# Kernel optimization log

Hardware: AMD Instinct MI355X
Metric: run time of the kernel (lower is better)

## Reference

```python
import jax, jax.numpy as jnp
import numpy as np

GS, GL, LS, LL, NA = 8, 8, 16, 8, 12
ALPHA = 0.5


def _rgb_to_lab(img):
    # img: (B,3,H,W) in [0,1]. Standard sRGB -> CIELab (kornia convention).
    lin = jnp.where(img > 0.04045, ((img + 0.055) / 1.055) ** 2.4, img / 12.92)
    r, g, b = lin[:, 0], lin[:, 1], lin[:, 2]
    x = 0.412453 * r + 0.357580 * g + 0.180423 * b
    y = 0.212671 * r + 0.715160 * g + 0.072169 * b
    z = 0.019334 * r + 0.119193 * g + 0.950227 * b
    xn, yn, zn = x / 0.950456, y, z / 1.088754
    f = lambda t: jnp.where(t > 0.008856, jnp.cbrt(t), 7.787 * t + 4.0 / 29.0)
    fx, fy, fz = f(xn), f(yn), f(zn)
    L = 116.0 * fy - 16.0
    a = 500.0 * (fx - fy)
    bb = 200.0 * (fy - fz)
    return L, a, bb


def _bilateral_slice(grid, img, guide):
    # grid: (B,12,s,s,l); img: (B,3,H,W); guide: (B,H,W) in [0,1]
    B, C, s, _, l = grid.shape
    _, _, H, W = img.shape
    g5 = jnp.transpose(grid, (0, 4, 2, 3, 1))  # (B, D=l, Hg=s, Wg=s, C)
    # align_corners=True coordinates, border padding == clamp
    fx = jnp.linspace(0.0, s - 1.0, W)                    # (W,)
    fy = jnp.linspace(0.0, s - 1.0, H)                    # (H,)
    fz = jnp.clip(guide * (l - 1.0), 0.0, l - 1.0)        # (B,H,W)
    x0 = jnp.floor(fx).astype(jnp.int32); x1 = jnp.minimum(x0 + 1, s - 1)
    y0 = jnp.floor(fy).astype(jnp.int32); y1 = jnp.minimum(y0 + 1, s - 1)
    z0 = jnp.floor(fz).astype(jnp.int32); z1 = jnp.minimum(z0 + 1, l - 1)
    wx = (fx - x0)[None, None, :, None]
    wy = (fy - y0)[None, :, None, None]
    wz = (fz - z0)[..., None]
    bi = jnp.arange(B)[:, None, None]
    yi0, yi1 = y0[None, :, None], y1[None, :, None]
    xi0, xi1 = x0[None, None, :], x1[None, None, :]

    def gat(zi, yi, xi):
        return g5[bi, zi, yi, xi]  # (B,H,W,C)

    def bilin(zi):
        c00 = gat(zi, yi0, xi0) * (1 - wx) + gat(zi, yi0, xi1) * wx
        c10 = gat(zi, yi1, xi0) * (1 - wx) + gat(zi, yi1, xi1) * wx
        return c00 * (1 - wy) + c10 * wy

    coeffs = bilin(z0) * (1 - wz) + bilin(z1) * wz       # (B,H,W,12)
    A = coeffs[..., :9].reshape(B, H, W, 3, 3)
    bvec = coeffs[..., 9:]
    img_hwc = jnp.transpose(img, (0, 2, 3, 1))           # (B,H,W,3)
    out = jnp.einsum('bhwck,bhwk->bhwc', A, img_hwc) + bvec
    return jnp.transpose(jnp.clip(out, 0.0, 1.0), (0, 3, 1, 2))


def setup_inputs() -> dict:
    key = jax.random.key(0)
    ks = jax.random.split(key, 16)
    B, H, W = 4, 896, 896
    n_h = n_w = 64
    inp = {
        'R_spatial': jax.random.normal(ks[0], (B, 256, n_h, n_w), jnp.float32),
        'F_sem': jax.random.normal(ks[1], (B, n_h * n_w, 384), jnp.float32),
        'img': jax.random.uniform(ks[2], (B, 3, H, W), jnp.float32),
        'n_h': n_h,
        'n_w': n_w,
    }
    sc = 0.02
    identity = np.array([1., 0., 0., 0., 1., 0., 0., 0., 1., 0., 0., 0.], np.float32)
    inp['dino_proj_w'] = jax.random.normal(ks[3], (128, 384), jnp.float32) * sc
    inp['dino_proj_b'] = jnp.zeros((128,), jnp.float32)
    inp['fusion_w'] = jax.random.normal(ks[4], (256, 384), jnp.float32) * sc
    inp['fusion_b'] = jnp.zeros((256,), jnp.float32)
    inp['g1_w'] = jax.random.normal(ks[5], (256, 256), jnp.float32) * sc
    inp['g1_b'] = jnp.zeros((256,), jnp.float32)
    inp['g2_w'] = jax.random.normal(ks[6], (NA * GS * GS * GL, 256), jnp.float32) * sc
    inp['g2_b'] = jnp.asarray(np.repeat(identity, GS * GS * GL))  # identity init
    inp['local_w'] = jax.random.normal(ks[7], (NA * LL, 256), jnp.float32) * sc
    inp['local_b'] = jnp.asarray(np.repeat(identity, LL))
    inp['guide_w1'] = jax.random.normal(ks[8], (64, 384), jnp.float32) * sc
    inp['guide_b1'] = jnp.zeros((64,), jnp.float32)
    inp['guide_w2'] = jax.random.normal(ks[9], (1, 64), jnp.float32) * sc
    inp['guide_b2'] = jnp.zeros((1,), jnp.float32)
    return inp


def reference(R_spatial, F_sem, img, n_h, n_w,
              dino_proj_w, dino_proj_b, fusion_w, fusion_b,
              g1_w, g1_b, g2_w, g2_b, local_w, local_b,
              guide_w1, guide_b1, guide_w2, guide_b2):
    B, _, H, W = img.shape
    # ---- GridNet ----
    F_sp = jnp.transpose(F_sem, (0, 2, 1)).reshape(B, 384, n_h, n_w)
    proj = jnp.einsum('bchw,oc->bohw', F_sp, dino_proj_w) + dino_proj_b[None, :, None, None]
    fused_in = jnp.concatenate([R_spatial, proj], axis=1)
    fused = jnp.einsum('bchw,oc->bohw', fused_in, fusion_w) + fusion_b[None, :, None, None]
    f_gap = fused.mean(axis=(-2, -1))                       # (B,256)
    h = jax.nn.relu(f_gap @ g1_w.T + g1_b)
    G_global = (h @ g2_w.T + g2_b).reshape(B, NA, GS, GS, GL)
    kh, kw = n_h // LS, n_w // LS
    pooled = fused.reshape(B, 256, LS, kh, LS, kw).mean(axis=(3, 5))
    lflat = jnp.einsum('bchw,oc->bohw', pooled, local_w) + local_b[None, :, None, None]
    G_local = jnp.transpose(lflat.reshape(B, NA, LL, LS, LS), (0, 1, 3, 4, 2))
    # ---- SemanticGuide ----
    L, a, bb = _rgb_to_lab(img)
    g_chroma = jnp.clip((0.5 * L + 0.25 * jnp.abs(a) + 0.25 * jnp.abs(bb)) / 114.0, 0.0, 1.0)
    hsem = jax.nn.relu(jnp.einsum('bnd,hd->bnh', F_sem, guide_w1) + guide_b1)
    g_sem_patch = jax.nn.sigmoid(jnp.einsum('bnh,oh->bno', hsem, guide_w2) + guide_b2)
    g_sem_patch = g_sem_patch.reshape(B, n_h, n_w, 1).transpose(0, 3, 1, 2)
    g_sem = jax.image.resize(g_sem_patch, (B, 1, H, W), 'bilinear')[:, 0]
    g = ALPHA * g_chroma + (1.0 - ALPHA) * g_sem
    # ---- slice + apply ----
    I_global = _bilateral_slice(G_global, img, g)
    I_local = _bilateral_slice(G_local, img, g)
    return I_global, I_local, G_global, G_local, g
```

## Files before the change

kernel.cpp:

```cpp
#include <hip/hip_runtime.h>
#include <math.h>

#define HWPIX 802816
#define OUT_IL 9633792
#define OUT_GG 19267584
#define OUT_GL 19292160
#define OUT_G  19390464

#define WS_WT4  0
#define WS_BC   163840
#define WS_POOL 164096
#define WS_H    426240
#define WS_GSEM 427264
#define WS_RG   443648
#define WS_RL   468224
#define WS_W1T  566528
#define WS_LWT  591104

__device__ __forceinline__ float fast_exp2(float x) {
  return __builtin_amdgcn_exp2f(x);
}
__device__ __forceinline__ float fast_log2(float x) {
  return __builtin_amdgcn_logf(x);
}
__device__ __forceinline__ float srgb_lin(float v) {
  float p = fast_exp2(2.4f * fast_log2((v + 0.055f) * (1.0f / 1.055f)));
  return v > 0.04045f ? p : v * (1.0f / 12.92f);
}
__device__ __forceinline__ float labf(float t) {
  float c = fast_exp2((1.0f / 3.0f) * fast_log2(t));
  return t > 0.008856f ? c : 7.787f * t + (4.0f / 29.0f);
}

__global__ __launch_bounds__(256) void k_prep(
    const float* __restrict__ fus_w, const float* __restrict__ fus_b,
    const float* __restrict__ dino_w, const float* __restrict__ dino_b,
    const float* __restrict__ gw1, const float* __restrict__ lw,
    float* __restrict__ Wt4, float* __restrict__ bc, float* __restrict__ w1T,
    float* __restrict__ lwT) {
  if (blockIdx.x == 642) {
    int t = threadIdx.x;
    for (int it = 0; it < 96; ++it) {
      int idx = it * 256 + t;
      int o = idx >> 8;
      int c = idx & 255;
      lwT[c * 96 + o] = lw[o * 256 + c];
    }
    return;
  }
  if (blockIdx.x == 641) {
    int t = threadIdx.x;
    for (int it = 0; it < 96; ++it) {
      int idx = it * 256 + t;
      int h = idx & 63;
      int k = idx >> 6;
      int kq = k / 96;
      int krem = k - kq * 96;
      int k4 = krem >> 2;
      int j = krem & 3;
      int hg = h >> 4, hl = h & 15;
      w1T[((((kq * 24 + k4) * 4 + hg) * 16) + hl) * 4 + j] = gw1[h * 384 + k];
    }
    return;
  }
  if (blockIdx.x == 640) {
    int o = threadIdx.x;
    float acc = fus_b[o];
    for (int m = 0; m < 128; ++m) acc += fus_w[o * 384 + 256 + m] * dino_b[m];
    bc[o] = acc;
    return;
  }
  int idx = blockIdx.x * 256 + threadIdx.x;
  int o = idx / 640;
  int k = idx - o * 640;
  float val;
  if (k < 256) {
    val = fus_w[o * 384 + k];
  } else {
    int d = k - 256;
    float acc = 0.0f;
    for (int m = 0; m < 128; ++m)
      acc += fus_w[o * 384 + 256 + m] * dino_w[m * 384 + d];
    val = acc;
  }
  Wt4[((k >> 2) * 256 + o) * 4 + (k & 3)] = val;
}

__global__ __launch_bounds__(1024) void k_fused_pool(
    const float* __restrict__ R, const float* __restrict__ F,
    const float* __restrict__ Wt4, const float* __restrict__ bc,
    const float* __restrict__ lwT, const float* __restrict__ lb,
    float* __restrict__ pooled, float* __restrict__ out4,
    float* __restrict__ rl) {
  int blk = blockIdx.x;
  int b = blk >> 6;
  int i = (blk >> 2) & 15;
  int jg = blk & 3;
  int t = threadIdx.x;
  int cell = t >> 8;
  int c = t & 255;
  __shared__ float s[4 * 640];
  {
    const float* rb = R + (((b * 256 + c) * 64 + i * 4) * 64) + (jg * 4 + cell) * 4;
    float p = 0.0f;
#pragma unroll
    for (int di = 0; di < 4; ++di) {
      float4 v = *(const float4*)(rb + di * 64);
      p += v.x + v.y + v.z + v.w;
    }
    s[cell * 640 + c] = p;
  }
  {
    float a0 = 0.0f, a1 = 0.0f;
    const float* fb = F + (size_t)(b * 4096 + (i * 4) * 64 + (jg * 4 + cell) * 4) * 384;
#pragma unroll
    for (int pix = 0; pix < 16; ++pix) {
      const float* fr = fb + (size_t)((pix >> 2) * 64 + (pix & 3)) * 384;
      a0 += fr[c];
      if (c < 128) a1 += fr[256 + c];
    }
    s[cell * 640 + 256 + c] = a0;
    if (c < 128) s[cell * 640 + 512 + c] = a1;
  }
  __syncthreads();
  float acc = 0.0f;
  const float4* w4 = (const float4*)Wt4;
  const float4* s4 = (const float4*)(s + cell * 640);
#pragma unroll 8
  for (int kk = 0; kk < 160; ++kk) {
    float4 wv = w4[kk * 256 + c];
    float4 sv = s4[kk];
    acc += wv.x * sv.x + wv.y * sv.y + wv.z * sv.z + wv.w * sv.w;
  }
  __syncthreads();
  s[cell * 256 + c] = acc;
  __syncthreads();
  if (t < 256) {
    float bco = bc[t];
    float4 v;
    v.x = s[0 * 256 + t] * (1.0f / 16.0f) + bco;
    v.y = s[1 * 256 + t] * (1.0f / 16.0f) + bco;
    v.z = s[2 * 256 + t] * (1.0f / 16.0f) + bco;
    v.w = s[3 * 256 + t] * (1.0f / 16.0f) + bco;
    *(float4*)(pooled + ((size_t)(b * 256 + t) * 256) + i * 16 + jg * 4) = v;
  } else if (t < 640) {
    int idx = t - 256;
    int cl = idx / 96;
    int o = idx - cl * 96;
    const float* sc_ = s + cl * 256;
    float acc2 = lb[o];
    for (int cc = 0; cc < 256; ++cc) {
      float pv = sc_[cc] * (1.0f / 16.0f) + bc[cc];
      acc2 += lwT[cc * 96 + o] * pv;
    }
    int cellg = i * 16 + jg * 4 + cl;
    int n = o >> 3, l = o & 7;
    out4[((b * 12 + n) * 256 + cellg) * 8 + l] = acc2;
    rl[b * 24576 + (cellg * 8 + l) * 12 + n] = acc2;
  }
}

__global__ __launch_bounds__(1024) void k_head(
    const float* __restrict__ pooled, const float* __restrict__ g1_w,
    const float* __restrict__ g1_b, const float* __restrict__ g2_w,
    const float* __restrict__ g2_b, float* __restrict__ out3,
    float* __restrict__ rg) {
  int b = blockIdx.x / 24;
  int og = (blockIdx.x % 24) * 256;
  int t = threadIdx.x;
  int ol = t & 255;
  int q = t >> 8;
  __shared__ float part[4][256];
  __shared__ float f[256];
  __shared__ float hv[256];
  {
    const float4* pr4 = (const float4*)(pooled + (size_t)(b * 256 + ol) * 256 + q * 64);
    float s = 0.0f;
#pragma unroll
    for (int i = 0; i < 16; ++i) {
      float4 v = pr4[i];
      s += v.x + v.y + v.z + v.w;
    }
    part[q][ol] = s;
  }
  __syncthreads();
  if (t < 256)
    f[t] = (part[0][t] + part[1][t] + part[2][t] + part[3][t]) * (1.0f / 256.0f);
  __syncthreads();
  {
    const float4* wr = (const float4*)(g1_w + (size_t)ol * 256 + q * 64);
    const float4* fq = (const float4*)(f + q * 64);
    float acc = 0.0f;
#pragma unroll
    for (int i = 0; i < 16; ++i) {
      float4 w = wr[i];
      float4 v = fq[i];
      acc += w.x * v.x + w.y * v.y + w.z * v.z + w.w * v.w;
    }
    part[q][ol] = acc;
  }
  __syncthreads();
  if (t < 256)
    hv[t] = fmaxf(part[0][t] + part[1][t] + part[2][t] + part[3][t] + g1_b[t], 0.0f);
  __syncthreads();
  {
    const float4* wr = (const float4*)(g2_w + (size_t)(og + ol) * 256 + q * 64);
    const float4* hq = (const float4*)(hv + q * 64);
    float acc = 0.0f;
#pragma unroll
    for (int i = 0; i < 16; ++i) {
      float4 w = wr[i];
      float4 v = hq[i];
      acc += w.x * v.x + w.y * v.y + w.z * v.z + w.w * v.w;
    }
    part[q][ol] = acc;
  }
  __syncthreads();
  if (t < 256) {
    int o = og + t;
    float a = part[0][t] + part[1][t] + part[2][t] + part[3][t] + g2_b[o];
    out3[b * 6144 + o] = a;
    int n = o >> 9, y = (o >> 6) & 7, x = (o >> 3) & 7, z = o & 7;
    rg[b * 6144 + ((y * 8 + x) * 8 + z) * 12 + n] = a;
  }
}

__global__ __launch_bounds__(256) void k_guide(
    const float* __restrict__ F, const float* __restrict__ w1T,
    const float* __restrict__ b1, const float* __restrict__ w2,
    const float* __restrict__ b2, float* __restrict__ gsem) {
  int t = threadIdx.x;
  int wave = t >> 6;
  int lane = t & 63;
  int kq = lane >> 4;
  int hl = lane & 15;
  int pb = blockIdx.x * 16;
  __shared__ float4 sF[16 * 4 * 25];
  const float4* Fb = (const float4*)(F + (size_t)pb * 384);
#pragma unroll
  for (int r6 = 0; r6 < 6; ++r6) {
    int g = r6 * 256 + t;
    int row = g / 96;
    int col = g - row * 96;
    int cq = col / 24;
    int c4 = col - cq * 24;
    sF[(row * 4 + cq) * 25 + c4] = Fb[g];
  }
  __syncthreads();
  float acc[4][4];
#pragma unroll
  for (int p = 0; p < 4; ++p)
#pragma unroll
    for (int hg = 0; hg < 4; ++hg) acc[p][hg] = 0.0f;
  const float4* w4 = (const float4*)w1T;
  int prow = wave * 4;
  for (int k4 = 0; k4 < 24; ++k4) {
    float4 wv0 = w4[((kq * 24 + k4) * 4 + 0) * 16 + hl];
    float4 wv1 = w4[((kq * 24 + k4) * 4 + 1) * 16 + hl];
    float4 wv2 = w4[((kq * 24 + k4) * 4 + 2) * 16 + hl];
    float4 wv3 = w4[((kq * 24 + k4) * 4 + 3) * 16 + hl];
#pragma unroll
    for (int p = 0; p < 4; ++p) {
      float4 fv = sF[((prow + p) * 4 + kq) * 25 + k4];
      acc[p][0] += fv.x * wv0.x + fv.y * wv0.y + fv.z * wv0.z + fv.w * wv0.w;
      acc[p][1] += fv.x * wv1.x + fv.y * wv1.y + fv.z * wv1.z + fv.w * wv1.w;
      acc[p][2] += fv.x * wv2.x + fv.y * wv2.y + fv.z * wv2.z + fv.w * wv2.w;
      acc[p][3] += fv.x * wv3.x + fv.y * wv3.y + fv.z * wv3.z + fv.w * wv3.w;
    }
  }
#pragma unroll
  for (int p = 0; p < 4; ++p)
#pragma unroll
    for (int hg = 0; hg < 4; ++hg) {
      float v = acc[p][hg];
      v += __shfl_xor(v, 16, 64);
      v += __shfl_xor(v, 32, 64);
      acc[p][hg] = v;
    }
  float b1v[4], w2v[4];
#pragma unroll
  for (int hg = 0; hg < 4; ++hg) {
    b1v[hg] = b1[hg * 16 + hl];
    w2v[hg] = w2[hg * 16 + hl];
  }
  float b2v = b2[0];
  float res = 0.0f;
#pragma unroll
  for (int p = 0; p < 4; ++p) {
    float v = 0.0f;
#pragma unroll
    for (int hg = 0; hg < 4; ++hg)
      v += fmaxf(acc[p][hg] + b1v[hg], 0.0f) * w2v[hg];
#pragma unroll
    for (int m = 8; m >= 1; m >>= 1) v += __shfl_xor(v, m, 64);
    if (lane == p) res = v;
  }
  if (lane < 4) gsem[pb + prow + lane] = 1.0f / (1.0f + expf(-(res + b2v)));
}

template <int SDIM>
__device__ __forceinline__ void slice_lds(
    const float* __restrict__ sg, int w, int z0, int z1, float wz,
    float r, float g, float bl, float& o0, float& o1, float& o2) {
  constexpr float sc = (float)(SDIM - 1) * (1.0f / 895.0f);
  float fxs = (float)w * sc;
  int x0 = (int)fxs;
  if (x0 > SDIM - 1) x0 = SDIM - 1;
  int x1 = x0 < SDIM - 1 ? x0 + 1 : SDIM - 1;
  float wx = fxs - (float)x0;
  float wz0 = 1.0f - wz;
  float w00 = (1.0f - wx) * wz0;
  float w01 = (1.0f - wx) * wz;
  float w10 = wx * wz0;
  float w11 = wx * wz;
  const float4* p00 = (const float4*)(sg + (x0 * 8 + z0) * 12);
  const float4* p01 = (const float4*)(sg + (x0 * 8 + z1) * 12);
  const float4* p10 = (const float4*)(sg + (x1 * 8 + z0) * 12);
  const float4* p11 = (const float4*)(sg + (x1 * 8 + z1) * 12);
  float a[12];
#pragma unroll
  for (int c = 0; c < 3; ++c) {
    float4 v00 = p00[c], v01 = p01[c], v10 = p10[c], v11 = p11[c];
    a[4 * c + 0] = w00 * v00.x + w01 * v01.x + w10 * v10.x + w11 * v11.x;
    a[4 * c + 1] = w00 * v00.y + w01 * v01.y + w10 * v10.y + w11 * v11.y;
    a[4 * c + 2] = w00 * v00.z + w01 * v01.z + w10 * v10.z + w11 * v11.z;
    a[4 * c + 3] = w00 * v00.w + w01 * v01.w + w10 * v10.w + w11 * v11.w;
  }
  o0 = fminf(fmaxf(a[0] * r + a[1] * g + a[2] * bl + a[9], 0.0f), 1.0f);
  o1 = fminf(fmaxf(a[3] * r + a[4] * g + a[5] * bl + a[10], 0.0f), 1.0f);
  o2 = fminf(fmaxf(a[6] * r + a[7] * g + a[8] * bl + a[11], 0.0f), 1.0f);
}

__global__ __launch_bounds__(448) void k_pixel(
    const float* __restrict__ img, const float* __restrict__ gsem,
    const float* __restrict__ rg, const float* __restrict__ rl,
    float* __restrict__ out) {
  int blk = blockIdx.x;
  int b = blk / 896;
  int h = blk - b * 896;
  int t = threadIdx.x;
  __shared__ float sgr[64];
  __shared__ float sG[768];
  __shared__ float sL[1536];

  int hwA = h * 896 + t;
  int hwB = hwA + 448;
  const float* imb = img + (size_t)b * 3 * HWPIX;
  float rrA = imb[hwA],             rrB = imb[hwB];
  float ggA = imb[HWPIX + hwA],     ggB = imb[HWPIX + hwB];
  float bbA = imb[2 * HWPIX + hwA], bbB = imb[2 * HWPIX + hwB];

  float sy = fminf(fmaxf((h + 0.5f) * (1.0f / 14.0f) - 0.5f, 0.0f), 63.0f);
  int y0s = (int)sy;
  int y1s = y0s < 63 ? y0s + 1 : 63;
  float wys = sy - (float)y0s;
  float fyg = (float)h * (7.0f / 895.0f);
  int y0g = (int)fyg;
  if (y0g > 7) y0g = 7;
  int y1g = y0g < 7 ? y0g + 1 : 7;
  float wyg = fyg - (float)y0g;
  float fyl = (float)h * (15.0f / 895.0f);
  int y0l = (int)fyl;
  if (y0l > 15) y0l = 15;
  int y1l = y0l < 15 ? y0l + 1 : 15;
  float wyl = fyl - (float)y0l;

  const float* g0 = rg + b * 6144 + y0g * 768;
  const float* g1 = rg + b * 6144 + y1g * 768;
  const float* l0 = rl + b * 24576 + y0l * 1536;
  const float* l1 = rl + b * 24576 + y1l * 1536;
  float ga0 = g0[t], gb0 = g1[t];
  float ga1 = 0.0f, gb1 = 0.0f;
  if (t < 320) { ga1 = g0[t + 448]; gb1 = g1[t + 448]; }
  float la0 = l0[t], lb0 = l1[t];
  float la1 = l0[t + 448], lb1 = l1[t + 448];
  float la2 = l0[t + 896], lb2s = l1[t + 896];
  float la3 = 0.0f, lb3 = 0.0f;
  if (t < 192) { la3 = l0[t + 1344]; lb3 = l1[t + 1344]; }
  float sg0 = 0.0f, sg1 = 0.0f;
  if (t < 64) {
    const float* gbp = gsem + b * 4096;
    sg0 = gbp[y0s * 64 + t];
    sg1 = gbp[y1s * 64 + t];
  }
  sG[t] = ga0 * (1.0f - wyg) + gb0 * wyg;
  if (t < 320) sG[t + 448] = ga1 * (1.0f - wyg) + gb1 * wyg;
  sL[t] = la0 * (1.0f - wyl) + lb0 * wyl;
  sL[t + 448] = la1 * (1.0f - wyl) + lb1 * wyl;
  sL[t + 896] = la2 * (1.0f - wyl) + lb2s * wyl;
  if (t < 192) sL[t + 1344] = la3 * (1.0f - wyl) + lb3 * wyl;
  if (t < 64) sgr[t] = sg0 * (1.0f - wys) + sg1 * wys;
  __syncthreads();

  float rr_[2] = {rrA, rrB}, gg_[2] = {ggA, ggB}, bb_[2] = {bbA, bbB};
#pragma unroll
  for (int ip = 0; ip < 2; ++ip) {
    int w = ip * 448 + t;
    int hw = h * 896 + w;
    float r = rr_[ip];
    float g = gg_[ip];
    float bl = bb_[ip];
    float lr = srgb_lin(r), lg = srgb_lin(g), lb2 = srgb_lin(bl);
    float X = 0.412453f * lr + 0.357580f * lg + 0.180423f * lb2;
    float Y = 0.212671f * lr + 0.715160f * lg + 0.072169f * lb2;
    float Z = 0.019334f * lr + 0.119193f * lg + 0.950227f * lb2;
    float fx_ = labf(X * (1.0f / 0.950456f));
    float fy_ = labf(Y);
    float fz_ = labf(Z * (1.0f / 1.088754f));
    float gch = 0.50877193f * fy_ - 0.070175439f +
                1.0964912f * fabsf(fx_ - fy_) + 0.43859649f * fabsf(fy_ - fz_);
    gch = fminf(fmaxf(gch, 0.0f), 1.0f);
    float sx = fminf(fmaxf((w + 0.5f) * (1.0f / 14.0f) - 0.5f, 0.0f), 63.0f);
    int x0s = (int)sx;
    int x1s = x0s < 63 ? x0s + 1 : 63;
    float wxs = sx - (float)x0s;
    float gs = sgr[x0s] * (1.0f - wxs) + sgr[x1s] * wxs;
    float gg = 0.5f * gch + 0.5f * gs;
    __builtin_nontemporal_store(gg, &out[OUT_G + b * HWPIX + hw]);
    float fzc = fminf(fmaxf(gg * 7.0f, 0.0f), 7.0f);
    int z0 = (int)fzc;
    if (z0 > 7) z0 = 7;
    int z1 = z0 < 7 ? z0 + 1 : 7;
    float wz = fzc - (float)z0;
    float o0, o1, o2;
    slice_lds<8>(sG, w, z0, z1, wz, r, g, bl, o0, o1, o2);
    __builtin_nontemporal_store(o0, &out[(b * 3 + 0) * HWPIX + hw]);
    __builtin_nontemporal_store(o1, &out[(b * 3 + 1) * HWPIX + hw]);
    __builtin_nontemporal_store(o2, &out[(b * 3 + 2) * HWPIX + hw]);
    slice_lds<16>(sL, w, z0, z1, wz, r, g, bl, o0, o1, o2);
    __builtin_nontemporal_store(o0, &out[OUT_IL + (b * 3 + 0) * HWPIX + hw]);
    __builtin_nontemporal_store(o1, &out[OUT_IL + (b * 3 + 1) * HWPIX + hw]);
    __builtin_nontemporal_store(o2, &out[OUT_IL + (b * 3 + 2) * HWPIX + hw]);
  }
}

extern "C" void kernel_launch(void* const* d_in, const int* in_sizes, int n_in,
                              void* d_out, int out_size, void* d_ws,
                              size_t ws_size, hipStream_t stream) {
  const float* R = (const float*)d_in[0];
  const float* F = (const float*)d_in[1];
  const float* img = (const float*)d_in[2];
  const float* dino_w = (const float*)d_in[5];
  const float* dino_b = (const float*)d_in[6];
  const float* fus_w = (const float*)d_in[7];
  const float* fus_b = (const float*)d_in[8];
  const float* g1_w = (const float*)d_in[9];
  const float* g1_b = (const float*)d_in[10];
  const float* g2_w = (const float*)d_in[11];
  const float* g2_b = (const float*)d_in[12];
  const float* lw = (const float*)d_in[13];
  const float* lb = (const float*)d_in[14];
  const float* gw1 = (const float*)d_in[15];
  const float* gb1 = (const float*)d_in[16];
  const float* gw2 = (const float*)d_in[17];
  const float* gb2 = (const float*)d_in[18];
  float* out = (float*)d_out;
  float* ws = (float*)d_ws;

  float* Wt4 = ws + WS_WT4;
  float* bc = ws + WS_BC;
  float* pooled = ws + WS_POOL;
  float* gsem = ws + WS_GSEM;
  float* rg = ws + WS_RG;
  float* rl = ws + WS_RL;
  float* w1T = ws + WS_W1T;
  float* lwT = ws + WS_LWT;

  k_prep<<<643, 256, 0, stream>>>(fus_w, fus_b, dino_w, dino_b, gw1, lw,
                                  Wt4, bc, w1T, lwT);
  k_guide<<<1024, 256, 0, stream>>>(F, w1T, gb1, gw2, gb2, gsem);
  k_fused_pool<<<256, 1024, 0, stream>>>(R, F, Wt4, bc, lwT, lb,
                                         pooled, out + OUT_GL, rl);
  k_head<<<96, 1024, 0, stream>>>(pooled, g1_w, g1_b, g2_w, g2_b,
                                  out + OUT_GG, rg);
  k_pixel<<<3584, 448, 0, stream>>>(img, gsem, rg, rl, out);
}
```

Before: 306.8 us.

## Merge guide MLP into fused-pool kernel with heterogeneous blocks

Folds the semantic-guide MLP kernel into the fused-pool kernel as extra blocks (768 blocks of 512 threads). Guide blocks now handle 32 patches each, and pool blocks use 512 threads that each process two cells and split the K loop in half, so every weight float4 is reused across all four cells. The pooled bias is applied once and stored in shared memory, so the local projection no longer recomputes it per element. This removes one launch and cuts weight reloads, but half the threads in guide blocks sit idle during compute.

```diff
diff --git a/kernel.cpp b/kernel.cpp
--- a/kernel.cpp
+++ b/kernel.cpp
@@ -10,7 +10,6 @@
 #define WS_WT4  0
 #define WS_BC   163840
 #define WS_POOL 164096
-#define WS_H    426240
 #define WS_GSEM 427264
 #define WS_RG   443648
 #define WS_RL   468224
@@ -86,77 +85,178 @@
   Wt4[((k >> 2) * 256 + o) * 4 + (k & 3)] = val;
 }
 
-__global__ __launch_bounds__(1024) void k_fused_pool(
+__global__ __launch_bounds__(512) void k_mid(
     const float* __restrict__ R, const float* __restrict__ F,
     const float* __restrict__ Wt4, const float* __restrict__ bc,
     const float* __restrict__ lwT, const float* __restrict__ lb,
     float* __restrict__ pooled, float* __restrict__ out4,
-    float* __restrict__ rl) {
+    float* __restrict__ rl,
+    const float* __restrict__ w1T, const float* __restrict__ b1,
+    const float* __restrict__ w2, const float* __restrict__ b2,
+    float* __restrict__ gsem) {
+  __shared__ float4 sbuf4[3200];
+  float* s = (float*)sbuf4;
   int blk = blockIdx.x;
+  int t = threadIdx.x;
+
+  if (blk >= 256) {
+    int gb = blk - 256;
+    int pb = gb * 32;
+    const float4* Fb = (const float4*)(F + (size_t)pb * 384);
+#pragma unroll
+    for (int r6 = 0; r6 < 6; ++r6) {
+      int g = r6 * 512 + t;
+      int row = g / 96;
+      int col = g - row * 96;
+      int cq = col / 24;
+      int c4 = col - cq * 24;
+      sbuf4[(row * 4 + cq) * 25 + c4] = Fb[g];
+    }
+    __syncthreads();
+    if (t < 256) {
+      int wave = t >> 6;
+      int lane = t & 63;
+      int kq = lane >> 4;
+      int hl = lane & 15;
+      float acc[8][4];
+#pragma unroll
+      for (int p = 0; p < 8; ++p)
+#pragma unroll
+        for (int hg = 0; hg < 4; ++hg) acc[p][hg] = 0.0f;
+      const float4* w4 = (const float4*)w1T;
+      int prow = wave * 8;
+      for (int k4 = 0; k4 < 24; ++k4) {
+        float4 wv0 = w4[((kq * 24 + k4) * 4 + 0) * 16 + hl];
+        float4 wv1 = w4[((kq * 24 + k4) * 4 + 1) * 16 + hl];
+        float4 wv2 = w4[((kq * 24 + k4) * 4 + 2) * 16 + hl];
+        float4 wv3 = w4[((kq * 24 + k4) * 4 + 3) * 16 + hl];
+#pragma unroll
+        for (int p = 0; p < 8; ++p) {
+          float4 fv = sbuf4[((prow + p) * 4 + kq) * 25 + k4];
+          acc[p][0] += fv.x * wv0.x + fv.y * wv0.y + fv.z * wv0.z + fv.w * wv0.w;
+          acc[p][1] += fv.x * wv1.x + fv.y * wv1.y + fv.z * wv1.z + fv.w * wv1.w;
+          acc[p][2] += fv.x * wv2.x + fv.y * wv2.y + fv.z * wv2.z + fv.w * wv2.w;
+          acc[p][3] += fv.x * wv3.x + fv.y * wv3.y + fv.z * wv3.z + fv.w * wv3.w;
+        }
+      }
+#pragma unroll
+      for (int p = 0; p < 8; ++p)
+#pragma unroll
+        for (int hg = 0; hg < 4; ++hg) {
+          float v = acc[p][hg];
+          v += __shfl_xor(v, 16, 64);
+          v += __shfl_xor(v, 32, 64);
+          acc[p][hg] = v;
+        }
+      float b1v[4], w2v[4];
+#pragma unroll
+      for (int hg = 0; hg < 4; ++hg) {
+        b1v[hg] = b1[hg * 16 + hl];
+        w2v[hg] = w2[hg * 16 + hl];
+      }
+      float b2v = b2[0];
+      float res = 0.0f;
+#pragma unroll
+      for (int p = 0; p < 8; ++p) {
+        float v = 0.0f;
+#pragma unroll
+        for (int hg = 0; hg < 4; ++hg)
+          v += fmaxf(acc[p][hg] + b1v[hg], 0.0f) * w2v[hg];
+#pragma unroll
+        for (int m = 8; m >= 1; m >>= 1) v += __shfl_xor(v, m, 64);
+        if (lane == p) res = v;
+      }
+      if (lane < 8) gsem[pb + prow + lane] = 1.0f / (1.0f + expf(-(res + b2v)));
+    }
+    return;
+  }
+
   int b = blk >> 6;
   int i = (blk >> 2) & 15;
   int jg = blk & 3;
-  int t = threadIdx.x;
-  int cell = t >> 8;
   int c = t & 255;
-  __shared__ float s[4 * 640];
+  int hp = t >> 8;
   {
-    const float* rb = R + (((b * 256 + c) * 64 + i * 4) * 64) + (jg * 4 + cell) * 4;
-    float p = 0.0f;
-#pragma unroll
-    for (int di = 0; di < 4; ++di) {
-      float4 v = *(const float4*)(rb + di * 64);
-      p += v.x + v.y + v.z + v.w;
-    }
-    s[cell * 640 + c] = p;
+#pragma unroll
+    for (int cl2 = 0; cl2 < 2; ++cl2) {
+      int cell = hp * 2 + cl2;
+      const float* rb = R + (((b * 256 + c) * 64 + i * 4) * 64) + (jg * 4 + cell) * 4;
+      float p = 0.0f;
+#pragma unroll
+      for (int di = 0; di < 4; ++di) {
+        float4 v = *(const float4*)(rb + di * 64);
+        p += v.x + v.y + v.z + v.w;
+      }
+      s[cell * 640 + c] = p;
+    }
   }
   {
-    float a0 = 0.0f, a1 = 0.0f;
-    const float* fb = F + (size_t)(b * 4096 + (i * 4) * 64 + (jg * 4 + cell) * 4) * 384;
-#pragma unroll
-    for (int pix = 0; pix < 16; ++pix) {
-      const float* fr = fb + (size_t)((pix >> 2) * 64 + (pix & 3)) * 384;
-      a0 += fr[c];
-      if (c < 128) a1 += fr[256 + c];
-    }
-    s[cell * 640 + 256 + c] = a0;
-    if (c < 128) s[cell * 640 + 512 + c] = a1;
-  }
-  __syncthreads();
-  float acc = 0.0f;
+#pragma unroll
+    for (int cl2 = 0; cl2 < 2; ++cl2) {
+      int cell = hp * 2 + cl2;
+      float a0 = 0.0f, a1 = 0.0f;
+      const float* fb = F + (size_t)(b * 4096 + (i * 4) * 64 + (jg * 4 + cell) * 4) * 384;
+#pragma unroll
+      for (int pix = 0; pix < 16; ++pix) {
+        const float* fr = fb + (size_t)((pix >> 2) * 64 + (pix & 3)) * 384;
+        a0 += fr[c];
+        if (c < 128) a1 += fr[256 + c];
+      }
+      s[cell * 640 + 256 + c] = a0;
+      if (c < 128) s[cell * 640 + 512 + c] = a1;
+    }
+  }
+  __syncthreads();
+  float acc0 = 0.0f, acc1 = 0.0f, acc2 = 0.0f, acc3 = 0.0f;
   const float4* w4 = (const float4*)Wt4;
-  const float4* s4 = (const float4*)(s + cell * 640);
+  const float4* s40 = (const float4*)(s + 0 * 640);
+  const float4* s41 = (const float4*)(s + 1 * 640);
+  const float4* s42 = (const float4*)(s + 2 * 640);
+  const float4* s43 = (const float4*)(s + 3 * 640);
+  int kk0 = hp * 80;
 #pragma unroll 8
-  for (int kk = 0; kk < 160; ++kk) {
+  for (int kk = kk0; kk < kk0 + 80; ++kk) {
     float4 wv = w4[kk * 256 + c];
-    float4 sv = s4[kk];
-    acc += wv.x * sv.x + wv.y * sv.y + wv.z * sv.z + wv.w * sv.w;
-  }
-  __syncthreads();
-  s[cell * 256 + c] = acc;
+    float4 v0 = s40[kk];
+    float4 v1 = s41[kk];
+    float4 v2 = s42[kk];
+    float4 v3 = s43[kk];
+    acc0 += wv.x * v0.x + wv.y * v0.y + wv.z * v0.z + wv.w * v0.w;
+    acc1 += wv.x * v1.x + wv.y * v1.y + wv.z * v1.z + wv.w * v1.w;
+    acc2 += wv.x * v2.x + wv.y * v2.y + wv.z * v2.z + wv.w * v2.w;
+    acc3 += wv.x * v3.x + wv.y * v3.y + wv.z * v3.z + wv.w * v3.w;
+  }
+  float* part = s + 2560;
+  part[(hp * 4 + 0) * 256 + c] = acc0;
+  part[(hp * 4 + 1) * 256 + c] = acc1;
+  part[(hp * 4 + 2) * 256 + c] = acc2;
+  part[(hp * 4 + 3) * 256 + c] = acc3;
   __syncthreads();
   if (t < 256) {
     float bco = bc[t];
-    float4 v;
-    v.x = s[0 * 256 + t] * (1.0f / 16.0f) + bco;
-    v.y = s[1 * 256 + t] * (1.0f / 16.0f) + bco;
-    v.z = s[2 * 256 + t] * (1.0f / 16.0f) + bco;
-    v.w = s[3 * 256 + t] * (1.0f / 16.0f) + bco;
+    float p0 = (part[(0 * 4 + 0) * 256 + t] + part[(1 * 4 + 0) * 256 + t]) * (1.0f / 16.0f) + bco;
+    float p1 = (part[(0 * 4 + 1) * 256 + t] + part[(1 * 4 + 1) * 256 + t]) * (1.0f / 16.0f) + bco;
+    float p2 = (part[(0 * 4 + 2) * 256 + t] + part[(1 * 4 + 2) * 256 + t]) * (1.0f / 16.0f) + bco;
+    float p3 = (part[(0 * 4 + 3) * 256 + t] + part[(1 * 4 + 3) * 256 + t]) * (1.0f / 16.0f) + bco;
+    float4 v = make_float4(p0, p1, p2, p3);
     *(float4*)(pooled + ((size_t)(b * 256 + t) * 256) + i * 16 + jg * 4) = v;
-  } else if (t < 640) {
-    int idx = t - 256;
-    int cl = idx / 96;
-    int o = idx - cl * 96;
+    s[0 * 256 + t] = p0;
+    s[1 * 256 + t] = p1;
+    s[2 * 256 + t] = p2;
+    s[3 * 256 + t] = p3;
+  }
+  __syncthreads();
+  if (t < 384) {
+    int cl = t / 96;
+    int o = t - cl * 96;
     const float* sc_ = s + cl * 256;
-    float acc2 = lb[o];
-    for (int cc = 0; cc < 256; ++cc) {
-      float pv = sc_[cc] * (1.0f / 16.0f) + bc[cc];
-      acc2 += lwT[cc * 96 + o] * pv;
-    }
+    float a2 = lb[o];
+    for (int cc = 0; cc < 256; ++cc)
+      a2 += lwT[cc * 96 + o] * sc_[cc];
     int cellg = i * 16 + jg * 4 + cl;
     int n = o >> 3, l = o & 7;
-    out4[((b * 12 + n) * 256 + cellg) * 8 + l] = acc2;
-    rl[b * 24576 + (cellg * 8 + l) * 12 + n] = acc2;
+    out4[((b * 12 + n) * 256 + cellg) * 8 + l] = a2;
+    rl[b * 24576 + (cellg * 8 + l) * 12 + n] = a2;
   }
 }
 
@@ -223,79 +323,6 @@
     int n = o >> 9, y = (o >> 6) & 7, x = (o >> 3) & 7, z = o & 7;
     rg[b * 6144 + ((y * 8 + x) * 8 + z) * 12 + n] = a;
   }
-}
-
-__global__ __launch_bounds__(256) void k_guide(
-    const float* __restrict__ F, const float* __restrict__ w1T,
-    const float* __restrict__ b1, const float* __restrict__ w2,
-    const float* __restrict__ b2, float* __restrict__ gsem) {
-  int t = threadIdx.x;
-  int wave = t >> 6;
-  int lane = t & 63;
-  int kq = lane >> 4;
-  int hl = lane & 15;
-  int pb = blockIdx.x * 16;
-  __shared__ float4 sF[16 * 4 * 25];
-  const float4* Fb = (const float4*)(F + (size_t)pb * 384);
-#pragma unroll
-  for (int r6 = 0; r6 < 6; ++r6) {
-    int g = r6 * 256 + t;
-    int row = g / 96;
-    int col = g - row * 96;
-    int cq = col / 24;
-    int c4 = col - cq * 24;
-    sF[(row * 4 + cq) * 25 + c4] = Fb[g];
-  }
-  __syncthreads();
-  float acc[4][4];
-#pragma unroll
-  for (int p = 0; p < 4; ++p)
-#pragma unroll
-    for (int hg = 0; hg < 4; ++hg) acc[p][hg] = 0.0f;
-  const float4* w4 = (const float4*)w1T;
-  int prow = wave * 4;
-  for (int k4 = 0; k4 < 24; ++k4) {
-    float4 wv0 = w4[((kq * 24 + k4) * 4 + 0) * 16 + hl];
-    float4 wv1 = w4[((kq * 24 + k4) * 4 + 1) * 16 + hl];
-    float4 wv2 = w4[((kq * 24 + k4) * 4 + 2) * 16 + hl];
-    float4 wv3 = w4[((kq * 24 + k4) * 4 + 3) * 16 + hl];
-#pragma unroll
-    for (int p = 0; p < 4; ++p) {
-      float4 fv = sF[((prow + p) * 4 + kq) * 25 + k4];
-      acc[p][0] += fv.x * wv0.x + fv.y * wv0.y + fv.z * wv0.z + fv.w * wv0.w;
-      acc[p][1] += fv.x * wv1.x + fv.y * wv1.y + fv.z * wv1.z + fv.w * wv1.w;
-      acc[p][2] += fv.x * wv2.x + fv.y * wv2.y + fv.z * wv2.z + fv.w * wv2.w;
-      acc[p][3] += fv.x * wv3.x + fv.y * wv3.y + fv.z * wv3.z + fv.w * wv3.w;
-    }
-  }
-#pragma unroll
-  for (int p = 0; p < 4; ++p)
-#pragma unroll
-    for (int hg = 0; hg < 4; ++hg) {
-      float v = acc[p][hg];
-      v += __shfl_xor(v, 16, 64);
-      v += __shfl_xor(v, 32, 64);
-      acc[p][hg] = v;
-    }
-  float b1v[4], w2v[4];
-#pragma unroll
-  for (int hg = 0; hg < 4; ++hg) {
-    b1v[hg] = b1[hg * 16 + hl];
-    w2v[hg] = w2[hg * 16 + hl];
-  }
-  float b2v = b2[0];
-  float res = 0.0f;
-#pragma unroll
-  for (int p = 0; p < 4; ++p) {
-    float v = 0.0f;
-#pragma unroll
-    for (int hg = 0; hg < 4; ++hg)
-      v += fmaxf(acc[p][hg] + b1v[hg], 0.0f) * w2v[hg];
-#pragma unroll
-    for (int m = 8; m >= 1; m >>= 1) v += __shfl_xor(v, m, 64);
-    if (lane == p) res = v;
-  }
-  if (lane < 4) gsem[pb + prow + lane] = 1.0f / (1.0f + expf(-(res + b2v)));
 }
 
 template <int SDIM>
@@ -468,9 +495,9 @@
 
   k_prep<<<643, 256, 0, stream>>>(fus_w, fus_b, dino_w, dino_b, gw1, lw,
                                   Wt4, bc, w1T, lwT);
-  k_guide<<<1024, 256, 0, stream>>>(F, w1T, gb1, gw2, gb2, gsem);
-  k_fused_pool<<<256, 1024, 0, stream>>>(R, F, Wt4, bc, lwT, lb,
-                                         pooled, out + OUT_GL, rl);
+  k_mid<<<768, 512, 0, stream>>>(R, F, Wt4, bc, lwT, lb,
+                                 pooled, out + OUT_GL, rl,
+                                 w1T, gb1, gw2, gb2, gsem);
   k_head<<<96, 1024, 0, stream>>>(pooled, g1_w, g1_b, g2_w, g2_b,
                                   out + OUT_GG, rg);
   k_pixel<<<3584, 448, 0, stream>>>(img, gsem, rg, rl, out);
```

Measured after the change: 300.9 us. Within noise of the previous version (-1.9%).
